# Performance work log

Hardware: AMD Instinct MI355X
Metric: run time of the kernel (lower is better)

## Reference

```python
import jax, jax.numpy as jnp
import numpy as np

D_MODEL = 1024
HEADS = 4
DK = 1024          # key_dim = d_model * expand_k
DV = 2048          # value_dim = d_model * expand_v
HDK = DK // HEADS  # 256
HDV = DV // HEADS  # 512
LOW_RANK = 16
CHUNK = 64
GATE_NORM = 16.0
EPS = 1e-5


def setup_inputs() -> dict:
    key = jax.random.key(0)
    ks = jax.random.split(key, 10)
    gain = 2.0 ** (-2.5)

    def xavier(k, shape):  # shape = (fan_in, fan_out); stored as [in, out]
        lim = gain * np.sqrt(6.0 / (shape[0] + shape[1]))
        return jax.random.uniform(k, shape, jnp.float32, -lim, lim)

    return {
        'x': jax.random.normal(ks[0], (2, 2048, D_MODEL), jnp.float32),
        'Wq': xavier(ks[1], (D_MODEL, DK)),
        'Wk': xavier(ks[2], (D_MODEL, DK)),
        'Wv': xavier(ks[3], (D_MODEL, DV)),
        'Wg': xavier(ks[4], (D_MODEL, DV)),
        'Wgk1': xavier(ks[5], (D_MODEL, LOW_RANK)),
        'Wgk2': xavier(ks[6], (LOW_RANK, DK)),
        'bgk2': jnp.zeros((DK,), jnp.float32),
        'Wo': xavier(ks[7], (DV, D_MODEL)),
        'rms_w': jnp.ones((HDV,), jnp.float32),
    }


def _gla_chunked(q, k, v, g):
    """Gated linear attention: S_t = exp(g_t) (*) S_{t-1} + k_t^T v_t;  o_t = scale * q_t @ S_t.
    q,k,g: [B,H,T,HDK]; v: [B,H,T,HDV]. Chunk-parallel formulation, scan over chunks."""
    B, H, T, _ = q.shape
    NC = T // CHUNK
    scale = HDK ** -0.5

    def to_chunks(t, d):  # [B,H,T,d] -> [NC,B,H,CHUNK,d]
        return t.reshape(B, H, NC, CHUNK, d).transpose(2, 0, 1, 3, 4)

    qc = to_chunks(q, HDK)
    kc = to_chunks(k, HDK)
    vc = to_chunks(v, HDV)
    bc = jnp.cumsum(to_chunks(g, HDK), axis=-2)  # inclusive log-decay within chunk
    mask = jnp.tril(jnp.ones((CHUNK, CHUNK), bool))

    def step(S, inp):
        qb, kb, vb, bb = inp                       # [B,H,C,HDK/HDV]
        qg = qb * jnp.exp(bb) * scale              # queries decayed to chunk start
        kd = kb * jnp.exp(-bb)                     # keys un-decayed (intra)
        A = jnp.einsum('bhtd,bhsd->bhts', qg, kd)  # intra-chunk scores
        A = jnp.where(mask, A, 0.0)
        o = jnp.einsum('bhts,bhsv->bhtv', A, vb) + jnp.einsum('bhtd,bhdv->bhtv', qg, S)
        b_last = bb[:, :, -1:, :]                  # [B,H,1,HDK]
        kg = kb * jnp.exp(b_last - bb)             # keys decayed to chunk end
        S = S * jnp.exp(b_last[:, :, 0, :])[..., None] + jnp.einsum('bhtd,bhtv->bhdv', kg, vb)
        return S, o

    S0 = jnp.zeros((B, H, HDK, HDV), q.dtype)
    _, o = jax.lax.scan(step, S0, (qc, kc, vc, bc))  # o: [NC,B,H,C,HDV]
    return o.transpose(1, 2, 0, 3, 4).reshape(B, H, T, HDV)


def reference(x, Wq, Wk, Wv, Wg, Wgk1, Wgk2, bgk2, Wo, rms_w):
    B, T, _ = x.shape
    q = (x @ Wq).reshape(B, T, HEADS, HDK).transpose(0, 2, 1, 3)
    k = (x @ Wk).reshape(B, T, HEADS, HDK).transpose(0, 2, 1, 3)
    v = (x @ Wv).reshape(B, T, HEADS, HDV).transpose(0, 2, 1, 3)
    gk = (x @ Wgk1) @ Wgk2 + bgk2                       # low-rank gate logits
    g = jax.nn.log_sigmoid(gk.astype(jnp.float32)) / GATE_NORM
    g = g.reshape(B, T, HEADS, HDK).transpose(0, 2, 1, 3)

    o = _gla_chunked(q, k, v, g)                        # [B,H,T,HDV]
    o = o.transpose(0, 2, 1, 3)                         # [B,T,H,HDV]
    o = o * jax.lax.rsqrt(jnp.mean(o * o, axis=-1, keepdims=True) + EPS) * rms_w
    o = o.reshape(B, T, HEADS * HDV)
    o = o * jax.nn.silu(x @ Wg)
    return o @ Wo
```

## Files before the change

### kernel.cpp

```cpp
#include <hip/hip_runtime.h>
#include <hip/hip_bf16.h>
#include <math.h>

#define TOK  4096
#define DM   1024
#define DKC  1024
#define DVC  2048
#define NH   4
#define HDK_ 256
#define HDV_ 512
#define NCH  32
#define CHK  64

typedef __attribute__((ext_vector_type(8))) short bf16x8;
typedef __attribute__((ext_vector_type(4))) float f32x4;

__device__ inline float bf2f(short s) {
    unsigned int b = ((unsigned int)(unsigned short)s) << 16;
    return __uint_as_float(b);
}
__device__ inline short f2bf_bits(float f) {
    __hip_bfloat16 h = __float2bfloat16(f);
    return *reinterpret_cast<short*>(&h);
}

__device__ __forceinline__ void gl_lds16(const void* g, void* l) {
    __builtin_amdgcn_global_load_lds((const __attribute__((address_space(1))) void*)g,
                                     (__attribute__((address_space(3))) void*)l, 16, 0, 0);
}

__global__ __launch_bounds__(256) void conv_bf16(const float* __restrict__ in,
                                                 __hip_bfloat16* __restrict__ out) {
    size_t i = ((size_t)blockIdx.x * 256 + threadIdx.x) * 4;
    float4 v = *reinterpret_cast<const float4*>(&in[i]);
    out[i + 0] = __float2bfloat16(v.x);
    out[i + 1] = __float2bfloat16(v.y);
    out[i + 2] = __float2bfloat16(v.z);
    out[i + 3] = __float2bfloat16(v.w);
}

__global__ __launch_bounds__(256) void convT(const float* __restrict__ W,
                                             __hip_bfloat16* __restrict__ Wt,
                                             int K, int N) {
    __shared__ float tile[32][33];
    int n0 = blockIdx.x * 32, k0 = blockIdx.y * 32;
    int tx = threadIdx.x & 31, ty = threadIdx.x >> 5;
#pragma unroll
    for (int i = 0; i < 32; i += 8)
        tile[ty + i][tx] = W[(size_t)(k0 + ty + i) * N + n0 + tx];
    __syncthreads();
#pragma unroll
    for (int i = 0; i < 32; i += 8)
        Wt[(size_t)(n0 + ty + i) * K + k0 + tx] = __float2bfloat16(tile[tx][ty + i]);
}

__global__ __launch_bounds__(256) void transpose_v(const __hip_bfloat16* __restrict__ v,
                                                   __hip_bfloat16* __restrict__ vT) {
    __shared__ short tile[32][33];
    const int tg0 = blockIdx.y * 32;
    const int vg0 = blockIdx.x * 32;
    const int tx = threadIdx.x & 31, ty = threadIdx.x >> 5;
    const short* vs = (const short*)v;
#pragma unroll
    for (int i = 0; i < 32; i += 8)
        tile[ty + i][tx] = vs[(size_t)(tg0 + ty + i) * DVC + vg0 + tx];
    __syncthreads();
    const int b = tg0 >> 11, tl0 = tg0 & 2047;
    const int h = vg0 >> 9, vl0 = vg0 & 511;
    const int bh = b * NH + h;
    short* vTs = (short*)vT;
#pragma unroll
    for (int i = 0; i < 32; i += 8)
        vTs[((size_t)bh * 512 + vl0 + ty + i) * 2048 + tl0 + tx] = tile[tx][ty + i];
}

__global__ __launch_bounds__(512) void gemm256(const __hip_bfloat16* __restrict__ A,
                                               const __hip_bfloat16* __restrict__ Wt,
                                               __hip_bfloat16* __restrict__ qo,
                                               __hip_bfloat16* __restrict__ ko,
                                               __hip_bfloat16* __restrict__ vo,
                                               __hip_bfloat16* __restrict__ xgo) {
    __shared__ __align__(16) short SM[9 * 8192];
    const int K = 1024, NT = 16;
    const int tid = threadIdx.x;
    const int wave = tid >> 6, lane = tid & 63;
    const int wr = wave >> 2;
    const int wc = wave & 3;
    const int hc = wc >> 1;
    const int l15 = lane & 15, kb = lane >> 4;
    const int m0 = blockIdx.y * 128, n0 = blockIdx.x * 256;

    __hip_bfloat16* dst; int ldd, nloc0;
    if (n0 < 1024)      { dst = qo;  ldd = 1024; nloc0 = n0; }
    else if (n0 < 2048) { dst = ko;  ldd = 1024; nloc0 = n0 - 1024; }
    else if (n0 < 4096) { dst = vo;  ldd = 2048; nloc0 = n0 - 2048; }
    else                { dst = xgo; ldd = 2048; nloc0 = n0 - 4096; }

    f32x4 acc[4][4];
#pragma unroll
    for (int mf = 0; mf < 4; ++mf)
#pragma unroll
        for (int nf = 0; nf < 4; ++nf) acc[mf][nf] = (f32x4){0.f, 0.f, 0.f, 0.f};

    auto stage_unit = [&](int u) {
        int tk = u / 3, p = u % 3;
        int slot = u % 9;
#pragma unroll
        for (int j = 0; j < 2; ++j) {
            int row = (wave * 2 + j) * 8 + (lane >> 3);
            int srcg = (lane & 7) ^ (row & 7);
            const __hip_bfloat16* src =
                (p == 0) ? &A[(size_t)(m0 + row) * K + tk * 64 + srcg * 8]
                         : &Wt[(size_t)(n0 + (p - 1) * 128 + row) * K + tk * 64 + srcg * 8];
            gl_lds16(src, &SM[slot * 8192 + (wave * 2 + j) * 512]);
        }
    };

    for (int u = 0; u <= 5; ++u) stage_unit(u);

    for (int t = 0; t < NT; ++t) {
        if (t < NT - 1) asm volatile("s_waitcnt vmcnt(6)" ::: "memory");
        else            asm volatile("s_waitcnt vmcnt(0)" ::: "memory");
        __builtin_amdgcn_sched_barrier(0);
        __builtin_amdgcn_s_barrier();

        {
            int u1 = 3 * t + 8;
            if (u1 > 3 * NT - 1) u1 = 3 * NT - 1;
            for (int u = 3 * t + 6; u <= u1; ++u) stage_unit(u);
        }

        const short* Abase = &SM[((3 * t) % 9) * 8192];
        const short* Bbase = &SM[((3 * t + 1 + hc) % 9) * 8192];
#pragma unroll
        for (int kk = 0; kk < 2; ++kk) {
            bf16x8 a[4], bfr[4];
#pragma unroll
            for (int mf = 0; mf < 4; ++mf) {
                int row = wr * 64 + mf * 16 + l15;
                int gsw = (kk * 4 + kb) ^ (row & 7);
                a[mf] = *reinterpret_cast<const bf16x8*>(&Abase[row * 64 + gsw * 8]);
            }
#pragma unroll
            for (int nf = 0; nf < 4; ++nf) {
                int row = (wc & 1) * 64 + nf * 16 + l15;
                int gsw = (kk * 4 + kb) ^ (row & 7);
                bfr[nf] = *reinterpret_cast<const bf16x8*>(&Bbase[row * 64 + gsw * 8]);
            }
            __builtin_amdgcn_s_setprio(1);
#pragma unroll
            for (int mf = 0; mf < 4; ++mf)
#pragma unroll
                for (int nf = 0; nf < 4; ++nf)
                    acc[mf][nf] = __builtin_amdgcn_mfma_f32_16x16x32_bf16(a[mf], bfr[nf], acc[mf][nf], 0, 0, 0);
            __builtin_amdgcn_s_setprio(0);
        }
    }

#pragma unroll
    for (int mf = 0; mf < 4; ++mf)
#pragma unroll
        for (int nf = 0; nf < 4; ++nf)
#pragma unroll
            for (int r = 0; r < 4; ++r)
                dst[(size_t)(m0 + wr * 64 + mf * 16 + kb * 4 + r) * ldd +
                    nloc0 + wc * 64 + nf * 16 + l15] = __float2bfloat16(acc[mf][nf][r]);
}

__global__ __launch_bounds__(256) void gemm_bf16(const __hip_bfloat16* __restrict__ A,
                                                 const __hip_bfloat16* __restrict__ Wt,
                                                 float* __restrict__ C,
                                                 int M, int N, int K) {
    __shared__ __align__(16) short Buf[2][2][128 * 64];
    const int tid = threadIdx.x;
    const int wave = tid >> 6, lane = tid & 63;
    const int wr = wave >> 1, wc = wave & 1;
    const int m0 = blockIdx.y * 128, n0 = blockIdx.x * 128;
    const int l15 = lane & 15, kb = lane >> 4;
    const int lr8 = lane >> 3, lc8 = (lane & 7) * 8;
    const int NT = K >> 6;

    f32x4 acc[4][4];
#pragma unroll
    for (int mf = 0; mf < 4; ++mf)
#pragma unroll
        for (int nf = 0; nf < 4; ++nf) acc[mf][nf] = (f32x4){0.f, 0.f, 0.f, 0.f};

#define STAGE_G(kt, bi)                                                          \
    {                                                                            \
        int k0s = (kt) * 64;                                                     \
        _Pragma("unroll")                                                        \
        for (int j = 0; j < 4; ++j) {                                            \
            int inst = wave * 4 + j;                                             \
            int r = inst * 8 + lr8;                                              \
            gl_lds16(&A[(size_t)(m0 + r) * K + k0s + lc8], &Buf[bi][0][inst * 512]); \
            gl_lds16(&Wt[(size_t)(n0 + r) * K + k0s + lc8], &Buf[bi][1][inst * 512]); \
        }                                                                        \
    }

    STAGE_G(0, 0);
    STAGE_G(1, 1);

    for (int t = 0; t < NT; ++t) {
        if (t + 1 < NT) asm volatile("s_waitcnt vmcnt(8)" ::: "memory");
        else            asm volatile("s_waitcnt vmcnt(0)" ::: "memory");
        __builtin_amdgcn_sched_barrier(0);
        __builtin_amdgcn_s_barrier();
        const short* Ab = Buf[t & 1][0];
        const short* Bb = Buf[t & 1][1];
#pragma unroll
        for (int kk = 0; kk < 2; ++kk) {
            bf16x8 af[4], bfr[4];
#pragma unroll
            for (int mf = 0; mf < 4; ++mf)
                af[mf] = *reinterpret_cast<const bf16x8*>(&Ab[(wr * 64 + mf * 16 + l15) * 64 + kk * 32 + kb * 8]);
#pragma unroll
            for (int nf = 0; nf < 4; ++nf)
                bfr[nf] = *reinterpret_cast<const bf16x8*>(&Bb[(wc * 64 + nf * 16 + l15) * 64 + kk * 32 + kb * 8]);
#pragma unroll
            for (int mf = 0; mf < 4; ++mf)
#pragma unroll
                for (int nf = 0; nf < 4; ++nf)
                    acc[mf][nf] = __builtin_amdgcn_mfma_f32_16x16x32_bf16(af[mf], bfr[nf], acc[mf][nf], 0, 0, 0);
        }
        asm volatile("s_waitcnt lgkmcnt(0)" ::: "memory");
        __builtin_amdgcn_sched_barrier(0);
        __builtin_amdgcn_s_barrier();
        if (t + 2 < NT) STAGE_G(t + 2, t & 1);
    }
#undef STAGE_G

#pragma unroll
    for (int mf = 0; mf < 4; ++mf)
#pragma unroll
        for (int nf = 0; nf < 4; ++nf)
#pragma unroll
            for (int r = 0; r < 4; ++r)
                C[(size_t)(m0 + wr * 64 + mf * 16 + kb * 4 + r) * N + n0 + wc * 64 + nf * 16 + l15] =
                    acc[mf][nf][r];
}

__global__ __launch_bounds__(256) void lowrank1(const float* __restrict__ x,
                                                const float* __restrict__ W1,
                                                float* __restrict__ t1) {
    __shared__ float red[16][17];
    const int t = blockIdx.x;
    const int tid = threadIdx.x;
    const int o = tid & 15;
    const int p = tid >> 4;
    float s = 0.f;
#pragma unroll 8
    for (int m = 0; m < 64; ++m) {
        int kk = p * 64 + m;
        s += x[(size_t)t * DM + kk] * W1[kk * 16 + o];
    }
    red[p][o] = s;
    __syncthreads();
    if (tid < 16) {
        float tot = 0.f;
#pragma unroll
        for (int pp = 0; pp < 16; ++pp) tot += red[pp][tid];
        t1[(size_t)t * 16 + tid] = tot;
    }
}

__global__ __launch_bounds__(256) void gate_k(const float* __restrict__ t1,
                                              const float* __restrict__ W2,
                                              const float* __restrict__ b2,
                                              float* __restrict__ g) {
    const size_t idx = (size_t)blockIdx.x * 256 + threadIdx.x;
    const int t = (int)(idx >> 10), c = (int)(idx & 1023);
    float acc = b2[c];
#pragma unroll
    for (int r = 0; r < 16; ++r) acc += t1[(size_t)t * 16 + r] * W2[r * 1024 + c];
    float ls = fminf(acc, 0.f) - log1pf(expf(-fabsf(acc)));
    g[idx] = ls * (1.f / 16.f);
}

__global__ __launch_bounds__(256) void gla_chunk(const __hip_bfloat16* __restrict__ qb,
                                                 const __hip_bfloat16* __restrict__ kb,
                                                 const __hip_bfloat16* __restrict__ vT,
                                                 const float* __restrict__ g,
                                                 __hip_bfloat16* __restrict__ qg,
                                                 __hip_bfloat16* __restrict__ kgT,
                                                 __hip_bfloat16* __restrict__ o1,
                                                 float* __restrict__ dlast) {
    __shared__ __align__(16) short SM[36864];
    short* qg_l = SM;
    short* kd_l = SM + 16384;
    short* V_l  = SM;
    short* Am_l = SM + 32768;

    const int chunk = blockIdx.x, bh = blockIdx.y;
    const int b = bh >> 2, h = bh & 3;
    const int t0 = b * 2048 + chunk * 64;
    const int tt0 = chunk * 64;
    const int tid = threadIdx.x;
    const float scale = 0.0625f;

    {
        const int d = tid;
        const float* gcol = g + (size_t)t0 * DKC + h * HDK_ + d;
        const __hip_bfloat16* qcol = qb + (size_t)t0 * DKC + h * HDK_ + d;
        const __hip_bfloat16* kcol = kb + (size_t)t0 * DKC + h * HDK_ + d;
        float run = 0.f;
#pragma unroll
        for (int i = 0; i < 64; ++i) run += gcol[(size_t)i * DKC];
        const float ebl = expf(run);
        dlast[((size_t)bh * NCH + chunk) * HDK_ + d] = ebl;

        bf16x8 kreg[8];
        run = 0.f;
#pragma unroll
        for (int i = 0; i < 64; ++i) {
            run += gcol[(size_t)i * DKC];
            float eb = expf(run);
            float qv = __bfloat162float(qcol[(size_t)i * DKC]) * eb * scale;
            float kdv = __bfloat162float(kcol[(size_t)i * DKC]) * expf(-run);
            qg[(size_t)(t0 + i) * DKC + h * HDK_ + d] = __float2bfloat16(qv);
            int bq = ((i * 512 + d * 2) ^ ((i & 7) << 4)) >> 1;
            qg_l[bq] = f2bf_bits(qv);
            kd_l[bq] = f2bf_bits(kdv);
            kreg[i >> 3][i & 7] = f2bf_bits(kdv * ebl);
        }
        __hip_bfloat16* kdst = kgT + ((size_t)(bh * HDK_ + d)) * 2048 + chunk * 64;
#pragma unroll
        for (int j = 0; j < 8; ++j)
            *reinterpret_cast<bf16x8*>(&kdst[j * 8]) = kreg[j];
    }
    __syncthreads();

    const int wv = tid >> 6, lane = tid & 63;
    const int l15 = lane & 15, kb_ = lane >> 4;

    {
        f32x4 accA[4];
#pragma unroll
        for (int sf = 0; sf < 4; ++sf) accA[sf] = (f32x4){0.f, 0.f, 0.f, 0.f};
        const int trow = wv * 16 + l15;
#pragma unroll
        for (int ks = 0; ks < 8; ++ks) {
            bf16x8 af = *reinterpret_cast<const bf16x8*>(
                &qg_l[((trow * 512 + (ks * 32 + kb_ * 8) * 2) ^ ((trow & 7) << 4)) >> 1]);
#pragma unroll
            for (int sf = 0; sf < 4; ++sf) {
                int srow = sf * 16 + l15;
                bf16x8 bfr = *reinterpret_cast<const bf16x8*>(
                    &kd_l[((srow * 512 + (ks * 32 + kb_ * 8) * 2) ^ ((srow & 7) << 4)) >> 1]);
                accA[sf] = __builtin_amdgcn_mfma_f32_16x16x32_bf16(af, bfr, accA[sf], 0, 0, 0);
            }
        }
#pragma unroll
        for (int sf = 0; sf < 4; ++sf)
#pragma unroll
            for (int r = 0; r < 4; ++r) {
                int t = wv * 16 + kb_ * 4 + r, s = sf * 16 + l15;
                float val = (t >= s) ? accA[sf][r] : 0.f;
                Am_l[((t * 128 + s * 2) ^ ((t & 7) << 4)) >> 1] = f2bf_bits(val);
            }
    }
    __syncthreads();

    {
        const int lr8 = lane >> 3, slot = lane & 7;
#pragma unroll
        for (int i8 = 0; i8 < 16; ++i8) {
            int vrow0 = wv * 128 + i8 * 8;
            const __hip_bfloat16* src =
                &vT[((size_t)bh * 512 + vrow0 + lr8) * 2048 + tt0 + (slot ^ (lr8 & 7)) * 8];
            gl_lds16(src, &V_l[vrow0 * 64]);
        }
    }
    __syncthreads();

    {
        f32x4 accO[4][8];
#pragma unroll
        for (int tf = 0; tf < 4; ++tf)
#pragma unroll
            for (int vf = 0; vf < 8; ++vf) accO[tf][vf] = (f32x4){0.f, 0.f, 0.f, 0.f};
#pragma unroll
        for (int kk = 0; kk < 2; ++kk) {
            bf16x8 af[4];
#pragma unroll
            for (int tf = 0; tf < 4; ++tf) {
                int row = tf * 16 + l15;
                af[tf] = *reinterpret_cast<const bf16x8*>(
                    &Am_l[((row * 128 + (kk * 32 + kb_ * 8) * 2) ^ ((row & 7) << 4)) >> 1]);
            }
#pragma unroll
            for (int vf = 0; vf < 8; ++vf) {
                int rv = wv * 128 + vf * 16 + l15;
                bf16x8 bfr = *reinterpret_cast<const bf16x8*>(
                    &V_l[((rv * 128 + (kk * 32 + kb_ * 8) * 2) ^ ((rv & 7) << 4)) >> 1]);
#pragma unroll
                for (int tf = 0; tf < 4; ++tf)
                    accO[tf][vf] = __builtin_amdgcn_mfma_f32_16x16x32_bf16(af[tf], bfr, accO[tf][vf], 0, 0, 0);
            }
        }
#pragma unroll
        for (int tf = 0; tf < 4; ++tf)
#pragma unroll
            for (int vf = 0; vf < 8; ++vf)
#pragma unroll
                for (int r = 0; r < 4; ++r) {
                    int t = tf * 16 + kb_ * 4 + r;
                    int vv = wv * 128 + vf * 16 + l15;
                    o1[(size_t)(t0 + t) * DVC + h * HDV_ + vv] = __float2bfloat16(accO[tf][vf][r]);
                }
    }
}

__global__ __launch_bounds__(256) void u_pass(const __hip_bfloat16* __restrict__ vT,
                                              const __hip_bfloat16* __restrict__ kgT,
                                              __hip_bfloat16* __restrict__ U) {
    __shared__ __align__(16) short Av[128 * 64];
    __shared__ __align__(16) short Bv[128 * 64];
    const int bx = blockIdx.x, c = blockIdx.y, bh = blockIdx.z;
    const int vc0 = (bx >> 1) * 128, d0 = (bx & 1) * 128;
    const int tid = threadIdx.x;
    const int wave = tid >> 6, lane = tid & 63;
    const int wr = wave >> 1, wc = wave & 1;
    const int l15 = lane & 15, kb = lane >> 4;
    const int lr8 = lane >> 3, lc8 = (lane & 7) * 8;

#pragma unroll
    for (int j = 0; j < 4; ++j) {
        int inst = wave * 4 + j;
        int r = inst * 8 + lr8;
        gl_lds16(&vT[((size_t)bh * 512 + vc0 + r) * 2048 + c * 64 + lc8], &Av[inst * 512]);
        gl_lds16(&kgT[((size_t)bh * HDK_ + d0 + r) * 2048 + c * 64 + lc8], &Bv[inst * 512]);
    }
    __syncthreads();

    f32x4 acc[4][4];
#pragma unroll
    for (int mf = 0; mf < 4; ++mf)
#pragma unroll
        for (int nf = 0; nf < 4; ++nf) acc[mf][nf] = (f32x4){0.f, 0.f, 0.f, 0.f};
#pragma unroll
    for (int kk = 0; kk < 2; ++kk) {
        bf16x8 af[4], bfr[4];
#pragma unroll
        for (int mf = 0; mf < 4; ++mf)
            af[mf] = *reinterpret_cast<const bf16x8*>(&Av[(wr * 64 + mf * 16 + l15) * 64 + kk * 32 + kb * 8]);
#pragma unroll
        for (int nf = 0; nf < 4; ++nf)
            bfr[nf] = *reinterpret_cast<const bf16x8*>(&Bv[(wc * 64 + nf * 16 + l15) * 64 + kk * 32 + kb * 8]);
#pragma unroll
        for (int mf = 0; mf < 4; ++mf)
#pragma unroll
            for (int nf = 0; nf < 4; ++nf)
                acc[mf][nf] = __builtin_amdgcn_mfma_f32_16x16x32_bf16(af[mf], bfr[nf], acc[mf][nf], 0, 0, 0);
    }
    const size_t Ub = ((size_t)bh * NCH + c) * 131072;
#pragma unroll
    for (int mf = 0; mf < 4; ++mf)
#pragma unroll
        for (int nf = 0; nf < 4; ++nf)
#pragma unroll
            for (int r = 0; r < 4; ++r) {
                int vc = vc0 + wr * 64 + mf * 16 + kb * 4 + r;
                int d = d0 + wc * 64 + nf * 16 + l15;
                U[Ub + (size_t)vc * 256 + d] = __float2bfloat16(acc[mf][nf][r]);
            }
}

__global__ __launch_bounds__(256) void scan_pass(__hip_bfloat16* __restrict__ U,
                                                 const float* __restrict__ dlast) {
    int gid = blockIdx.x * 256 + threadIdx.x;
    int bh = gid >> 14;
    int rem = gid & 16383;
    int vc = rem >> 5;
    int dg = rem & 31;
    float S[8];
#pragma unroll
    for (int j = 0; j < 8; ++j) S[j] = 0.f;
    size_t base = (size_t)bh * NCH * 131072 + (size_t)vc * 256 + dg * 8;
    for (int c = 0; c < NCH; ++c) {
        __hip_bfloat16* p = U + base + (size_t)c * 131072;
        bf16x8 u = *reinterpret_cast<bf16x8*>(p);
        const float* dl = &dlast[((size_t)bh * NCH + c) * HDK_ + dg * 8];
        float4 e0 = *reinterpret_cast<const float4*>(dl);
        float4 e1 = *reinterpret_cast<const float4*>(dl + 4);
        float e[8] = {e0.x, e0.y, e0.z, e0.w, e1.x, e1.y, e1.z, e1.w};
        bf16x8 outv;
#pragma unroll
        for (int j = 0; j < 8; ++j) {
            outv[j] = f2bf_bits(S[j]);
            S[j] = S[j] * e[j] + bf2f(u[j]);
        }
        *reinterpret_cast<bf16x8*>(p) = outv;
    }
}

__global__ __launch_bounds__(256) void o_pass(const __hip_bfloat16* __restrict__ qg,
                                              const __hip_bfloat16* __restrict__ U,
                                              const __hip_bfloat16* __restrict__ o1,
                                              __hip_bfloat16* __restrict__ o2) {
    __shared__ __align__(16) char smem[64 * 132 * 4];
    short* Av = (short*)smem;
    short* Bv = (short*)smem + 128 * 64;
    float* oT = (float*)smem;
    const int vt = blockIdx.x, c = blockIdx.y, bh = blockIdx.z;
    const int b = bh >> 2, h = bh & 3;
    const int vc0 = vt * 128;
    const int t0 = b * 2048 + c * 64;
    const int tid = threadIdx.x;
    const int wave = tid >> 6, lane = tid & 63;
    const int wr = wave >> 1, wc = wave & 1;
    const int l15 = lane & 15, kb = lane >> 4;
    const int lr8 = lane >> 3, lc8 = (lane & 7) * 8;
    const size_t Ub = ((size_t)bh * NCH + c) * 131072;

    f32x4 acc[4][2];
#pragma unroll
    for (int mf = 0; mf < 4; ++mf)
#pragma unroll
        for (int nf = 0; nf < 2; ++nf) acc[mf][nf] = (f32x4){0.f, 0.f, 0.f, 0.f};

    for (int ks = 0; ks < 4; ++ks) {
        const int d0 = ks * 64;
#pragma unroll
        for (int j = 0; j < 4; ++j) {
            int inst = wave * 4 + j;
            int r = inst * 8 + lr8;
            gl_lds16(&U[Ub + (size_t)(vc0 + r) * 256 + d0 + lc8], &Av[inst * 512]);
        }
#pragma unroll
        for (int j = 0; j < 2; ++j) {
            int inst = wave * 2 + j;
            int r = inst * 8 + lr8;
            gl_lds16(&qg[(size_t)(t0 + r) * DKC + h * HDK_ + d0 + lc8], &Bv[inst * 512]);
        }
        __syncthreads();
#pragma unroll
        for (int kk = 0; kk < 2; ++kk) {
            bf16x8 af[4], bfr[2];
#pragma unroll
            for (int mf = 0; mf < 4; ++mf)
                af[mf] = *reinterpret_cast<const bf16x8*>(&Av[(wr * 64 + mf * 16 + l15) * 64 + kk * 32 + kb * 8]);
#pragma unroll
            for (int nf = 0; nf < 2; ++nf)
                bfr[nf] = *reinterpret_cast<const bf16x8*>(&Bv[(wc * 32 + nf * 16 + l15) * 64 + kk * 32 + kb * 8]);
#pragma unroll
            for (int mf = 0; mf < 4; ++mf)
#pragma unroll
                for (int nf = 0; nf < 2; ++nf)
                    acc[mf][nf] = __builtin_amdgcn_mfma_f32_16x16x32_bf16(af[mf], bfr[nf], acc[mf][nf], 0, 0, 0);
        }
        __syncthreads();
    }
#pragma unroll
    for (int mf = 0; mf < 4; ++mf)
#pragma unroll
        for (int nf = 0; nf < 2; ++nf)
#pragma unroll
            for (int r = 0; r < 4; ++r)
                oT[(wc * 32 + nf * 16 + l15) * 132 + wr * 64 + mf * 16 + kb * 4 + r] = acc[mf][nf][r];
    __syncthreads();
#pragma unroll
    for (int j = 0; j < 4; ++j) {
        int t = (tid >> 4) + j * 16;
        int vc8 = (tid & 15) * 8;
        float4 a0 = *reinterpret_cast<const float4*>(&oT[t * 132 + vc8]);
        float4 a1 = *reinterpret_cast<const float4*>(&oT[t * 132 + vc8 + 4]);
        size_t oi = (size_t)(t0 + t) * DVC + h * HDV_ + vc0 + vc8;
        bf16x8 iv = *reinterpret_cast<const bf16x8*>(&o1[oi]);
        bf16x8 outv;
        outv[0] = f2bf_bits(a0.x + bf2f(iv[0]));
        outv[1] = f2bf_bits(a0.y + bf2f(iv[1]));
        outv[2] = f2bf_bits(a0.z + bf2f(iv[2]));
        outv[3] = f2bf_bits(a0.w + bf2f(iv[3]));
        outv[4] = f2bf_bits(a1.x + bf2f(iv[4]));
        outv[5] = f2bf_bits(a1.y + bf2f(iv[5]));
        outv[6] = f2bf_bits(a1.z + bf2f(iv[6]));
        outv[7] = f2bf_bits(a1.w + bf2f(iv[7]));
        *reinterpret_cast<bf16x8*>((__hip_bfloat16*)o2 + oi) = outv;
    }
}

__global__ __launch_bounds__(256) void rms_gate(const __hip_bfloat16* __restrict__ o2,
                                                const __hip_bfloat16* __restrict__ xg,
                                                const float* __restrict__ rms_w,
                                                __hip_bfloat16* __restrict__ gated) {
    __shared__ float wsum[4];
    const int th = blockIdx.x;
    const int t = th >> 2, h = th & 3;
    const int tid = threadIdx.x;
    const size_t base = (size_t)t * DVC + h * HDV_;
    short2 ov = reinterpret_cast<const short2*>((const short*)o2 + base)[tid];
    float v0 = bf2f(ov.x), v1 = bf2f(ov.y);
    float s = v0 * v0 + v1 * v1;
#pragma unroll
    for (int off = 32; off >= 1; off >>= 1) s += __shfl_down(s, off, 64);
    if ((tid & 63) == 0) wsum[tid >> 6] = s;
    __syncthreads();
    float tot = wsum[0] + wsum[1] + wsum[2] + wsum[3];
    float rms = rsqrtf(tot * (1.f / 512.f) + 1e-5f);
    short2 gv = reinterpret_cast<const short2*>((const short*)xg + base)[tid];
    float g0 = bf2f(gv.x), g1 = bf2f(gv.y);
    float s0 = g0 / (1.f + expf(-g0));
    float s1 = g1 / (1.f + expf(-g1));
    float2 w = reinterpret_cast<const float2*>(rms_w)[tid];
    short2 outp;
    outp.x = f2bf_bits(v0 * rms * w.x * s0);
    outp.y = f2bf_bits(v1 * rms * w.y * s1);
    reinterpret_cast<short2*>((short*)gated + base)[tid] = outp;
}

extern "C" void kernel_launch(void* const* d_in, const int* in_sizes, int n_in,
                              void* d_out, int out_size, void* d_ws, size_t ws_size,
                              hipStream_t stream) {
    const float* x    = (const float*)d_in[0];
    const float* Wq   = (const float*)d_in[1];
    const float* Wk   = (const float*)d_in[2];
    const float* Wv   = (const float*)d_in[3];
    const float* Wg   = (const float*)d_in[4];
    const float* Wgk1 = (const float*)d_in[5];
    const float* Wgk2 = (const float*)d_in[6];
    const float* bgk2 = (const float*)d_in[7];
    const float* Wo   = (const float*)d_in[8];
    const float* rmsw = (const float*)d_in[9];
    float* out = (float*)d_out;
    float* ws = (float*)d_ws;

    const size_t M1 = 1ull << 20;
    __hip_bfloat16* xb    = (__hip_bfloat16*)ws;
    __hip_bfloat16* WtAll = (__hip_bfloat16*)(ws + 2 * M1);
    __hip_bfloat16* q_b   = (__hip_bfloat16*)(ws + 5 * M1);
    __hip_bfloat16* k_b   = (__hip_bfloat16*)(ws + 7 * M1);
    __hip_bfloat16* v_b   = (__hip_bfloat16*)(ws + 9 * M1);
    float*          g     = ws + 13 * M1;
    __hip_bfloat16* U     = (__hip_bfloat16*)ws;
    __hip_bfloat16* xg_b  = (__hip_bfloat16*)(ws + 17 * M1);
    __hip_bfloat16* qgb   = (__hip_bfloat16*)(ws + 21 * M1);
    __hip_bfloat16* kgT   = (__hip_bfloat16*)(ws + 23 * M1);
    __hip_bfloat16* vT    = (__hip_bfloat16*)(ws + 25 * M1);
    __hip_bfloat16* o1    = (__hip_bfloat16*)(ws + 29 * M1);
    __hip_bfloat16* o2    = (__hip_bfloat16*)(ws + 33 * M1);
    float*          t1    = ws + 37 * M1;
    float*          dlast = ws + 37 * M1 + 65536;
    __hip_bfloat16* WtO   = (__hip_bfloat16*)(ws + 23 * M1);
    __hip_bfloat16* gated = (__hip_bfloat16*)(ws + 25 * M1);

    conv_bf16<<<4096, 256, 0, stream>>>(x, xb);
    convT<<<dim3(32, 32), 256, 0, stream>>>(Wq, WtAll,                    DM, DKC);
    convT<<<dim3(32, 32), 256, 0, stream>>>(Wk, WtAll + 1024 * 1024,      DM, DKC);
    convT<<<dim3(64, 32), 256, 0, stream>>>(Wv, WtAll + 2048 * 1024,      DM, DVC);
    convT<<<dim3(64, 32), 256, 0, stream>>>(Wg, WtAll + 4096 * 1024,      DM, DVC);

    gemm256<<<dim3(24, 32), 512, 0, stream>>>(xb, WtAll, q_b, k_b, v_b, xg_b);

    transpose_v<<<dim3(64, 128), 256, 0, stream>>>(v_b, vT);
    lowrank1<<<TOK, 256, 0, stream>>>(x, Wgk1, t1);
    gate_k<<<(TOK * DKC) / 256, 256, 0, stream>>>(t1, Wgk2, bgk2, g);
    gla_chunk<<<dim3(NCH, 8), 256, 0, stream>>>(q_b, k_b, vT, g, qgb, kgT, o1, dlast);

    u_pass<<<dim3(8, NCH, 8), 256, 0, stream>>>(vT, kgT, U);
    scan_pass<<<512, 256, 0, stream>>>(U, dlast);
    o_pass<<<dim3(4, NCH, 8), 256, 0, stream>>>(qgb, U, o1, o2);

    convT<<<dim3(32, 64), 256, 0, stream>>>(Wo, WtO, DVC, DM);
    rms_gate<<<TOK * NH, 256, 0, stream>>>(o2, xg_b, rmsw, gated);
    gemm_bf16<<<dim3(8, 32), 256, 0, stream>>>(gated, WtO, out, TOK, DM, DVC);
}
```

Baseline: 272.2 us.

## Fuse x conversion with gate computation; write V transposed from the GEMM epilogue

Merges the bf16 conversion of x, the low-rank projection and the gate log-sigmoid into one per-token kernel, so x is read once and the t1 intermediate is never written. The projection GEMM now transposes V tiles through LDS in its epilogue and writes vT directly, which removes the separate transpose_v kernel and its round trip of V through global memory. Three kernel launches are dropped. In exchange the V-tile blocks gain extra LDS traffic and barriers, and the gate matmul now runs per token inside one block.

```diff
diff --git a/kernel.cpp b/kernel.cpp
--- a/kernel.cpp
+++ b/kernel.cpp
@@ -29,14 +29,48 @@
                                      (__attribute__((address_space(3))) void*)l, 16, 0, 0);
 }
 
-__global__ __launch_bounds__(256) void conv_bf16(const float* __restrict__ in,
-                                                 __hip_bfloat16* __restrict__ out) {
-    size_t i = ((size_t)blockIdx.x * 256 + threadIdx.x) * 4;
-    float4 v = *reinterpret_cast<const float4*>(&in[i]);
-    out[i + 0] = __float2bfloat16(v.x);
-    out[i + 1] = __float2bfloat16(v.y);
-    out[i + 2] = __float2bfloat16(v.z);
-    out[i + 3] = __float2bfloat16(v.w);
+__global__ __launch_bounds__(256) void prep_x(const float* __restrict__ x,
+                                              const float* __restrict__ W1,
+                                              const float* __restrict__ W2,
+                                              const float* __restrict__ b2,
+                                              __hip_bfloat16* __restrict__ xb,
+                                              float* __restrict__ g) {
+    __shared__ float xl[1024];
+    __shared__ float red[16][17];
+    __shared__ float t1l[16];
+    const int t = blockIdx.x, tid = threadIdx.x;
+    float4 xv = *reinterpret_cast<const float4*>(&x[(size_t)t * DM + tid * 4]);
+    *reinterpret_cast<float4*>(&xl[tid * 4]) = xv;
+    short4 xs;
+    xs.x = f2bf_bits(xv.x); xs.y = f2bf_bits(xv.y);
+    xs.z = f2bf_bits(xv.z); xs.w = f2bf_bits(xv.w);
+    *reinterpret_cast<short4*>((short*)xb + (size_t)t * DM + tid * 4) = xs;
+    __syncthreads();
+    const int o = tid & 15, p = tid >> 4;
+    float s = 0.f;
+#pragma unroll 8
+    for (int m = 0; m < 64; ++m) {
+        int kk = p * 64 + m;
+        s += xl[kk] * W1[kk * 16 + o];
+    }
+    red[p][o] = s;
+    __syncthreads();
+    if (tid < 16) {
+        float tot = 0.f;
+#pragma unroll
+        for (int pp = 0; pp < 16; ++pp) tot += red[pp][tid];
+        t1l[tid] = tot;
+    }
+    __syncthreads();
+#pragma unroll
+    for (int j = 0; j < 4; ++j) {
+        int c = tid + j * 256;
+        float acc = b2[c];
+#pragma unroll
+        for (int r = 0; r < 16; ++r) acc += t1l[r] * W2[r * 1024 + c];
+        float ls = fminf(acc, 0.f) - log1pf(expf(-fabsf(acc)));
+        g[(size_t)t * DKC + c] = ls * (1.f / 16.f);
+    }
 }
 
 __global__ __launch_bounds__(256) void convT(const float* __restrict__ W,
@@ -54,31 +88,11 @@
         Wt[(size_t)(n0 + ty + i) * K + k0 + tx] = __float2bfloat16(tile[tx][ty + i]);
 }
 
-__global__ __launch_bounds__(256) void transpose_v(const __hip_bfloat16* __restrict__ v,
-                                                   __hip_bfloat16* __restrict__ vT) {
-    __shared__ short tile[32][33];
-    const int tg0 = blockIdx.y * 32;
-    const int vg0 = blockIdx.x * 32;
-    const int tx = threadIdx.x & 31, ty = threadIdx.x >> 5;
-    const short* vs = (const short*)v;
-#pragma unroll
-    for (int i = 0; i < 32; i += 8)
-        tile[ty + i][tx] = vs[(size_t)(tg0 + ty + i) * DVC + vg0 + tx];
-    __syncthreads();
-    const int b = tg0 >> 11, tl0 = tg0 & 2047;
-    const int h = vg0 >> 9, vl0 = vg0 & 511;
-    const int bh = b * NH + h;
-    short* vTs = (short*)vT;
-#pragma unroll
-    for (int i = 0; i < 32; i += 8)
-        vTs[((size_t)bh * 512 + vl0 + ty + i) * 2048 + tl0 + tx] = tile[tx][ty + i];
-}
-
 __global__ __launch_bounds__(512) void gemm256(const __hip_bfloat16* __restrict__ A,
                                                const __hip_bfloat16* __restrict__ Wt,
                                                __hip_bfloat16* __restrict__ qo,
                                                __hip_bfloat16* __restrict__ ko,
-                                               __hip_bfloat16* __restrict__ vo,
+                                               __hip_bfloat16* __restrict__ vT,
                                                __hip_bfloat16* __restrict__ xgo) {
     __shared__ __align__(16) short SM[9 * 8192];
     const int K = 1024, NT = 16;
@@ -90,11 +104,11 @@
     const int l15 = lane & 15, kb = lane >> 4;
     const int m0 = blockIdx.y * 128, n0 = blockIdx.x * 256;
 
-    __hip_bfloat16* dst; int ldd, nloc0;
-    if (n0 < 1024)      { dst = qo;  ldd = 1024; nloc0 = n0; }
-    else if (n0 < 2048) { dst = ko;  ldd = 1024; nloc0 = n0 - 1024; }
-    else if (n0 < 4096) { dst = vo;  ldd = 2048; nloc0 = n0 - 2048; }
-    else                { dst = xgo; ldd = 2048; nloc0 = n0 - 4096; }
+    const bool isV = (n0 >= 2048 && n0 < 4096);
+    __hip_bfloat16* dst = nullptr; int ldd = 0, nloc0 = 0;
+    if (n0 < 1024)       { dst = qo;  ldd = 1024; nloc0 = n0; }
+    else if (n0 < 2048)  { dst = ko;  ldd = 1024; nloc0 = n0 - 1024; }
+    else if (n0 >= 4096) { dst = xgo; ldd = 2048; nloc0 = n0 - 4096; }
 
     f32x4 acc[4][4];
 #pragma unroll
@@ -157,14 +171,44 @@
         }
     }
 
-#pragma unroll
-    for (int mf = 0; mf < 4; ++mf)
-#pragma unroll
-        for (int nf = 0; nf < 4; ++nf)
-#pragma unroll
-            for (int r = 0; r < 4; ++r)
-                dst[(size_t)(m0 + wr * 64 + mf * 16 + kb * 4 + r) * ldd +
-                    nloc0 + wc * 64 + nf * 16 + l15] = __float2bfloat16(acc[mf][nf][r]);
+    if (!isV) {
+#pragma unroll
+        for (int mf = 0; mf < 4; ++mf)
+#pragma unroll
+            for (int nf = 0; nf < 4; ++nf)
+#pragma unroll
+                for (int r = 0; r < 4; ++r)
+                    dst[(size_t)(m0 + wr * 64 + mf * 16 + kb * 4 + r) * ldd +
+                        nloc0 + wc * 64 + nf * 16 + l15] = __float2bfloat16(acc[mf][nf][r]);
+    } else {
+        __syncthreads();
+        short* Cl = SM;
+#pragma unroll
+        for (int mf = 0; mf < 4; ++mf)
+#pragma unroll
+            for (int nf = 0; nf < 4; ++nf)
+#pragma unroll
+                for (int r = 0; r < 4; ++r) {
+                    int trow = wr * 64 + mf * 16 + kb * 4 + r;
+                    int vcol = wc * 64 + nf * 16 + l15;
+                    Cl[vcol * 132 + trow] = f2bf_bits(acc[mf][nf][r]);
+                }
+        __syncthreads();
+        const int vcg0 = n0 - 2048;
+        const int bh = (m0 >> 11) * NH + (vcg0 >> 9);
+        const int vl0 = vcg0 & 511;
+        const int tl0 = m0 & 2047;
+        short* vTs = (short*)vT;
+#pragma unroll
+        for (int it = 0; it < 8; ++it) {
+            int idx = tid + it * 512;
+            int row = idx >> 4;
+            int c8 = (idx & 15) * 8;
+            bf16x8 vv = *reinterpret_cast<const bf16x8*>(&Cl[row * 132 + c8]);
+            *reinterpret_cast<bf16x8*>(
+                &vTs[((size_t)(bh * 512 + vl0 + row)) * 2048 + tl0 + c8]) = vv;
+        }
+    }
 }
 
 __global__ __launch_bounds__(256) void gemm_bf16(const __hip_bfloat16* __restrict__ A,
@@ -238,43 +282,6 @@
             for (int r = 0; r < 4; ++r)
                 C[(size_t)(m0 + wr * 64 + mf * 16 + kb * 4 + r) * N + n0 + wc * 64 + nf * 16 + l15] =
                     acc[mf][nf][r];
-}
-
-__global__ __launch_bounds__(256) void lowrank1(const float* __restrict__ x,
-                                                const float* __restrict__ W1,
-                                                float* __restrict__ t1) {
-    __shared__ float red[16][17];
-    const int t = blockIdx.x;
-    const int tid = threadIdx.x;
-    const int o = tid & 15;
-    const int p = tid >> 4;
-    float s = 0.f;
-#pragma unroll 8
-    for (int m = 0; m < 64; ++m) {
-        int kk = p * 64 + m;
-        s += x[(size_t)t * DM + kk] * W1[kk * 16 + o];
-    }
-    red[p][o] = s;
-    __syncthreads();
-    if (tid < 16) {
-        float tot = 0.f;
-#pragma unroll
-        for (int pp = 0; pp < 16; ++pp) tot += red[pp][tid];
-        t1[(size_t)t * 16 + tid] = tot;
-    }
-}
-
-__global__ __launch_bounds__(256) void gate_k(const float* __restrict__ t1,
-                                              const float* __restrict__ W2,
-                                              const float* __restrict__ b2,
-                                              float* __restrict__ g) {
-    const size_t idx = (size_t)blockIdx.x * 256 + threadIdx.x;
-    const int t = (int)(idx >> 10), c = (int)(idx & 1023);
-    float acc = b2[c];
-#pragma unroll
-    for (int r = 0; r < 16; ++r) acc += t1[(size_t)t * 16 + r] * W2[r * 1024 + c];
-    float ls = fminf(acc, 0.f) - log1pf(expf(-fabsf(acc)));
-    g[idx] = ls * (1.f / 16.f);
 }
 
 __global__ __launch_bounds__(256) void gla_chunk(const __hip_bfloat16* __restrict__ qb,
@@ -630,7 +637,6 @@
     __hip_bfloat16* WtAll = (__hip_bfloat16*)(ws + 2 * M1);
     __hip_bfloat16* q_b   = (__hip_bfloat16*)(ws + 5 * M1);
     __hip_bfloat16* k_b   = (__hip_bfloat16*)(ws + 7 * M1);
-    __hip_bfloat16* v_b   = (__hip_bfloat16*)(ws + 9 * M1);
     float*          g     = ws + 13 * M1;
     __hip_bfloat16* U     = (__hip_bfloat16*)ws;
     __hip_bfloat16* xg_b  = (__hip_bfloat16*)(ws + 17 * M1);
@@ -639,22 +645,18 @@
     __hip_bfloat16* vT    = (__hip_bfloat16*)(ws + 25 * M1);
     __hip_bfloat16* o1    = (__hip_bfloat16*)(ws + 29 * M1);
     __hip_bfloat16* o2    = (__hip_bfloat16*)(ws + 33 * M1);
-    float*          t1    = ws + 37 * M1;
     float*          dlast = ws + 37 * M1 + 65536;
     __hip_bfloat16* WtO   = (__hip_bfloat16*)(ws + 23 * M1);
     __hip_bfloat16* gated = (__hip_bfloat16*)(ws + 25 * M1);
 
-    conv_bf16<<<4096, 256, 0, stream>>>(x, xb);
+    prep_x<<<TOK, 256, 0, stream>>>(x, Wgk1, Wgk2, bgk2, xb, g);
     convT<<<dim3(32, 32), 256, 0, stream>>>(Wq, WtAll,                    DM, DKC);
     convT<<<dim3(32, 32), 256, 0, stream>>>(Wk, WtAll + 1024 * 1024,      DM, DKC);
     convT<<<dim3(64, 32), 256, 0, stream>>>(Wv, WtAll + 2048 * 1024,      DM, DVC);
     convT<<<dim3(64, 32), 256, 0, stream>>>(Wg, WtAll + 4096 * 1024,      DM, DVC);
 
-    gemm256<<<dim3(24, 32), 512, 0, stream>>>(xb, WtAll, q_b, k_b, v_b, xg_b);
-
-    transpose_v<<<dim3(64, 128), 256, 0, stream>>>(v_b, vT);
-    lowrank1<<<TOK, 256, 0, stream>>>(x, Wgk1, t1);
-    gate_k<<<(TOK * DKC) / 256, 256, 0, stream>>>(t1, Wgk2, bgk2, g);
+    gemm256<<<dim3(24, 32), 512, 0, stream>>>(xb, WtAll, q_b, k_b, vT, xg_b);
+
     gla_chunk<<<dim3(NCH, 8), 256, 0, stream>>>(q_b, k_b, vT, g, qgb, kgT, o1, dlast);
 
     u_pass<<<dim3(8, NCH, 8), 256, 0, stream>>>(vT, kgT, U);
```

Measured after the change: 250.9 us. 7.8% less time.
